# Kernel optimization log

Hardware: AMD Instinct MI355X
Metric: run time of the kernel (lower is better)

## Reference

```python
import jax, jax.numpy as jnp
import numpy as np

N_NODES = 50000


def _gcn_norm(edge_index):
    # symmetric GCN normalization 1/sqrt(deg_src*deg_dst), computed from edge list
    src, dst = edge_index[0], edge_index[1]
    ones = jnp.ones(src.shape[0], dtype=jnp.float32)
    deg = jax.ops.segment_sum(ones, dst, num_segments=N_NODES)
    deg = jnp.maximum(deg, 1.0)
    inv_sqrt = jax.lax.rsqrt(deg)
    return inv_sqrt[src] * inv_sqrt[dst]  # [E]


def _graph_conv(x, src, dst, norm, W, b):
    # gather messages from source nodes, normalize, scatter-add to destinations
    msgs = x[src] * norm[:, None]                       # [E, F]
    agg = jax.ops.segment_sum(msgs, dst, num_segments=N_NODES)  # [N, F]
    return agg @ W + b


def setup_inputs() -> dict:
    key = jax.random.key(0)
    ks = jax.random.split(key, 8)
    F, H, C, E = 128, 256, 40, 600000
    x = jax.random.normal(ks[0], (N_NODES, F), dtype=jnp.float32)
    edge_index = jax.random.randint(ks[1], (2, E), 0, N_NODES, dtype=jnp.int32)
    W1 = jax.random.normal(ks[2], (F, H), dtype=jnp.float32) * (1.0 / np.sqrt(F))
    b1 = jnp.zeros((H,), dtype=jnp.float32)
    W2 = jax.random.normal(ks[3], (H, H), dtype=jnp.float32) * (1.0 / np.sqrt(H))
    b2 = jnp.zeros((H,), dtype=jnp.float32)
    Wd = jax.random.normal(ks[4], (H, C), dtype=jnp.float32) * (1.0 / np.sqrt(H))
    bd = jnp.zeros((C,), dtype=jnp.float32)
    return {"x": x, "edge_index": edge_index, "W1": W1, "b1": b1,
            "W2": W2, "b2": b2, "Wd": Wd, "bd": bd}


def reference(x, edge_index, W1, b1, W2, b2, Wd, bd):
    src, dst = edge_index[0], edge_index[1]
    norm = _gcn_norm(edge_index)
    h = jax.nn.relu(_graph_conv(x, src, dst, norm, W1, b1))
    h = jax.nn.relu(_graph_conv(h, src, dst, norm, W2, b2))
    return jax.nn.softmax(h @ Wd + bd, axis=-1)
```

## Files before the change

### kernel.cpp

```cpp
#include <hip/hip_runtime.h>
#include <hip/hip_bf16.h>
#include <math.h>

#define N_NODES 50000

typedef short short8 __attribute__((ext_vector_type(8)));
typedef float f32x4 __attribute__((ext_vector_type(4)));

static __device__ __forceinline__ void split2(float x, unsigned short& hi, unsigned short& lo) {
    unsigned u = __builtin_bit_cast(unsigned, x);
    unsigned r = u + 0x7FFF + ((u >> 16) & 1);
    hi = (unsigned short)(r >> 16);
    float hf = __builtin_bit_cast(float, (unsigned)hi << 16);
    float res = x - hf;
    unsigned v = __builtin_bit_cast(unsigned, res);
    unsigned r2 = v + 0x7FFF + ((v >> 16) & 1);
    lo = (unsigned short)(r2 >> 16);
}


__global__ void deg_kernel(const int* __restrict__ dst, int* __restrict__ deg, int E) {
    int e = blockIdx.x * blockDim.x + threadIdx.x;
    if (e < E) atomicAdd(&deg[dst[e]], 1);
}


__global__ void scan_p1(const int* __restrict__ deg, int* __restrict__ bsum, int n) {
    int t = threadIdx.x;
    int base = blockIdx.x * 1024 + t * 4;
    int4 v = make_int4(0, 0, 0, 0);
    if (base + 3 < n) v = *(const int4*)(deg + base);
    else {
        if (base + 0 < n) v.x = deg[base + 0];
        if (base + 1 < n) v.y = deg[base + 1];
        if (base + 2 < n) v.z = deg[base + 2];
    }
    int s = v.x + v.y + v.z + v.w;
    #pragma unroll
    for (int off = 32; off > 0; off >>= 1) s += __shfl_xor(s, off);
    __shared__ int wpart[4];
    if ((t & 63) == 0) wpart[t >> 6] = s;
    __syncthreads();
    if (t == 0) bsum[blockIdx.x] = wpart[0] + wpart[1] + wpart[2] + wpart[3];
}

__global__ void scan_p2(int* __restrict__ bsum, int nb, int* __restrict__ rowptr, int n) {
    int t = threadIdx.x;
    int v = (t < nb) ? bsum[t] : 0;
    int sc = v;
    #pragma unroll
    for (int off = 1; off < 64; off <<= 1) {
        int u = __shfl_up(sc, off);
        if (t >= off) sc += u;
    }
    if (t < nb) bsum[t] = sc - v;
    if (t == 63) rowptr[n] = sc;
}

__global__ void scan_p3(const int* __restrict__ deg, const int* __restrict__ bsum,
                        int* __restrict__ rowptr, int* __restrict__ cursor,
                        float* __restrict__ inv, int n) {
    int t = threadIdx.x;
    int base = blockIdx.x * 1024 + t * 4;
    int4 v = make_int4(0, 0, 0, 0);
    if (base + 3 < n) v = *(const int4*)(deg + base);
    else {
        if (base + 0 < n) v.x = deg[base + 0];
        if (base + 1 < n) v.y = deg[base + 1];
        if (base + 2 < n) v.z = deg[base + 2];
    }
    int s = v.x + v.y + v.z + v.w;
    int lane = t & 63;
    int sc = s;
    #pragma unroll
    for (int off = 1; off < 64; off <<= 1) {
        int u = __shfl_up(sc, off);
        if (lane >= off) sc += u;
    }
    __shared__ int wpart[4], woff[4];
    if (lane == 63) wpart[t >> 6] = sc;
    __syncthreads();
    if (t == 0) { int a = 0; for (int i = 0; i < 4; ++i) { woff[i] = a; a += wpart[i]; } }
    __syncthreads();
    int run = bsum[blockIdx.x] + woff[t >> 6] + (sc - s);
    if (base + 0 < n) { rowptr[base + 0] = run; cursor[base + 0] = run; run += v.x; inv[base + 0] = rsqrtf(fmaxf((float)v.x, 1.0f)); }
    if (base + 1 < n) { rowptr[base + 1] = run; cursor[base + 1] = run; run += v.y; inv[base + 1] = rsqrtf(fmaxf((float)v.y, 1.0f)); }
    if (base + 2 < n) { rowptr[base + 2] = run; cursor[base + 2] = run; run += v.z; inv[base + 2] = rsqrtf(fmaxf((float)v.z, 1.0f)); }
    if (base + 3 < n) { rowptr[base + 3] = run; cursor[base + 3] = run; run += v.w; inv[base + 3] = rsqrtf(fmaxf((float)v.w, 1.0f)); }
}


__global__ void fill_kernel(const int* __restrict__ src, const int* __restrict__ dst,
                            const float* __restrict__ inv, int* __restrict__ cursor,
                            int* __restrict__ src_s, float* __restrict__ norm_s, int E) {
    int e = blockIdx.x * blockDim.x + threadIdx.x;
    if (e >= E) return;
    int s = src[e];
    int d = dst[e];
    int pos = atomicAdd(&cursor[d], 1);
    src_s[pos] = s;
    norm_s[pos] = inv[s] * inv[d];
}


__global__ void gather_agg_pass(const float* __restrict__ x, int coff, int ss,
                                const int* __restrict__ rowptr, const int* __restrict__ src_s,
                                const float* __restrict__ norm_s,
                                unsigned short* __restrict__ agg_hi,
                                unsigned short* __restrict__ agg_lo, int as) {
    int node = blockIdx.x * 4 + (threadIdx.x >> 6);
    if (node >= N_NODES) return;
    int lane = threadIdx.x & 63;
    int beg = rowptr[node];
    int end = rowptr[node + 1];
    const float* xb = x + coff + (size_t)lane * 2;

    float2 acc = {0.0f, 0.0f};
    int p = beg;
    for (; p + 4 <= end; p += 4) {
        int s0 = src_s[p], s1 = src_s[p + 1], s2 = src_s[p + 2], s3 = src_s[p + 3];
        float n0 = norm_s[p], n1 = norm_s[p + 1], n2 = norm_s[p + 2], n3 = norm_s[p + 3];
        float2 v0 = *(const float2*)(xb + (size_t)s0 * ss);
        float2 v1 = *(const float2*)(xb + (size_t)s1 * ss);
        float2 v2 = *(const float2*)(xb + (size_t)s2 * ss);
        float2 v3 = *(const float2*)(xb + (size_t)s3 * ss);
        acc.x = fmaf(v0.x, n0, acc.x); acc.y = fmaf(v0.y, n0, acc.y);
        acc.x = fmaf(v1.x, n1, acc.x); acc.y = fmaf(v1.y, n1, acc.y);
        acc.x = fmaf(v2.x, n2, acc.x); acc.y = fmaf(v2.y, n2, acc.y);
        acc.x = fmaf(v3.x, n3, acc.x); acc.y = fmaf(v3.y, n3, acc.y);
    }
    for (; p < end; ++p) {
        int s0 = src_s[p];
        float n0 = norm_s[p];
        float2 v0 = *(const float2*)(xb + (size_t)s0 * ss);
        acc.x = fmaf(v0.x, n0, acc.x);
        acc.y = fmaf(v0.y, n0, acc.y);
    }

    unsigned short h0, l0, h1, l1;
    split2(acc.x, h0, l0);
    split2(acc.y, h1, l1);
    unsigned hp = (unsigned)h0 | ((unsigned)h1 << 16);
    unsigned lp = (unsigned)l0 | ((unsigned)l1 << 16);
    size_t o = (size_t)node * as + coff + (size_t)lane * 2;
    *(unsigned*)(agg_hi + o) = hp;
    *(unsigned*)(agg_lo + o) = lp;
}


__global__ void split_w_all(const float* __restrict__ W1, const float* __restrict__ W2,
                            unsigned short* __restrict__ w1hi, unsigned short* __restrict__ w1lo,
                            unsigned short* __restrict__ w2hi, unsigned short* __restrict__ w2lo) {
    int i = blockIdx.x * 256 + threadIdx.x;
    if (i < 128 * 256) {
        int k = i >> 8;
        int n = i & 255;
        unsigned short h, l;
        split2(W1[i], h, l);
        w1hi[(size_t)n * 128 + k] = h;
        w1lo[(size_t)n * 128 + k] = l;
    } else {
        int j = i - 128 * 256;
        int k = j >> 8;
        int n = j & 255;
        unsigned short h, l;
        split2(W2[j], h, l);
        w2hi[(size_t)n * 256 + k] = h;
        w2lo[(size_t)n * 256 + k] = l;
    }
}


template<int K, bool RELU>
__global__ __launch_bounds__(256) void gemm_mfma_kernel(
    const unsigned short* __restrict__ Ahi, const unsigned short* __restrict__ Alo,
    const unsigned short* __restrict__ Bhi, const unsigned short* __restrict__ Blo,
    const float* __restrict__ bias, float* __restrict__ out, int M)
{
    constexpr int LDA = 40;
    __shared__ unsigned short AsH[2][64][LDA];
    __shared__ unsigned short AsL[2][64][LDA];

    int tid = threadIdx.x;
    int lane = tid & 63;
    int wave = tid >> 6;
    int row0 = blockIdx.x * 64;
    int col0 = wave * 64;
    int lr = lane & 15;
    int koff0 = (lane >> 4) * 8;

    int srow = tid >> 2;
    int skg = (tid & 3) << 3;

    f32x4 acc[4][4];
    #pragma unroll
    for (int i = 0; i < 4; ++i)
        #pragma unroll
        for (int j = 0; j < 4; ++j) acc[i][j] = (f32x4){0.f, 0.f, 0.f, 0.f};

    short8 rh, rl;
    rh = *(const short8*)(Ahi + (size_t)(row0 + srow) * K + skg);
    rl = *(const short8*)(Alo + (size_t)(row0 + srow) * K + skg);
    *(short8*)&AsH[0][srow][skg] = rh;
    *(short8*)&AsL[0][srow][skg] = rl;
    __syncthreads();

    constexpr int NT = K / 32;
    #pragma unroll 1
    for (int t = 0; t < NT; ++t) {
        int cur = t & 1;
        int ko = t * 32 + koff0;

        short8 bh[4], bl[4];
        #pragma unroll
        for (int q = 0; q < 4; ++q) {
            size_t boff = (size_t)(col0 + q * 16 + lr) * K + ko;
            bh[q] = *(const short8*)(Bhi + boff);
            bl[q] = *(const short8*)(Blo + boff);
        }

        if (t + 1 < NT) {
            int kk = (t + 1) * 32;
            rh = *(const short8*)(Ahi + (size_t)(row0 + srow) * K + kk + skg);
            rl = *(const short8*)(Alo + (size_t)(row0 + srow) * K + kk + skg);
        }

        short8 ah[4], al[4];
        #pragma unroll
        for (int q = 0; q < 4; ++q) {
            ah[q] = *(const short8*)&AsH[cur][q * 16 + lr][koff0];
            al[q] = *(const short8*)&AsL[cur][q * 16 + lr][koff0];
        }

        #pragma unroll
        for (int mt = 0; mt < 4; ++mt)
            #pragma unroll
            for (int nt = 0; nt < 4; ++nt) {
                acc[mt][nt] = __builtin_amdgcn_mfma_f32_16x16x32_bf16(ah[mt], bh[nt], acc[mt][nt], 0, 0, 0);
                acc[mt][nt] = __builtin_amdgcn_mfma_f32_16x16x32_bf16(ah[mt], bl[nt], acc[mt][nt], 0, 0, 0);
                acc[mt][nt] = __builtin_amdgcn_mfma_f32_16x16x32_bf16(al[mt], bh[nt], acc[mt][nt], 0, 0, 0);
            }

        if (t + 1 < NT) {
            *(short8*)&AsH[cur ^ 1][srow][skg] = rh;
            *(short8*)&AsL[cur ^ 1][srow][skg] = rl;
        }
        __syncthreads();
    }

    int rgrp = (lane >> 4) * 4;
    #pragma unroll
    for (int mt = 0; mt < 4; ++mt) {
        #pragma unroll
        for (int nt = 0; nt < 4; ++nt) {
            int c = col0 + nt * 16 + lr;
            float bv = bias[c];
            #pragma unroll
            for (int reg = 0; reg < 4; ++reg) {
                int r = row0 + mt * 16 + rgrp + reg;
                if (r < M) {
                    float v = acc[mt][nt][reg] + bv;
                    if (RELU) v = fmaxf(v, 0.0f);
                    out[(size_t)r * 256 + c] = v;
                }
            }
        }
    }
}


__global__ __launch_bounds__(256) void dense_softmax_kernel(const float* __restrict__ h,
                                                            const float* __restrict__ Wd,
                                                            const float* __restrict__ bd,
                                                            float* __restrict__ out, int M) {
    __shared__ float hs[32][260];
    __shared__ float wt[40][260];
    int tid = threadIdx.x;
    int row0 = blockIdx.x * 32;

    for (int i = tid; i < 40 * 256; i += 256) {
        int k = i / 40;
        int c = i - k * 40;
        wt[c][k] = Wd[i];
    }
    #pragma unroll
    for (int i = 0; i < 8; ++i) {
        int f = tid + i * 256;
        int r = f >> 6;
        int k4 = (f & 63) << 2;
        float4 v = make_float4(0.f, 0.f, 0.f, 0.f);
        if (row0 + r < M) v = *(const float4*)(h + (size_t)(row0 + r) * 256 + k4);
        *(float4*)&hs[r][k4] = v;
    }
    __syncthreads();

    int r  = tid >> 3;
    int cg = tid & 7;
    int c0 = cg * 5;

    float acc[5] = {0.f, 0.f, 0.f, 0.f, 0.f};
    #pragma unroll 4
    for (int k4 = 0; k4 < 64; ++k4) {
        float4 hv = *(float4*)&hs[r][k4 * 4];
        #pragma unroll
        for (int j = 0; j < 5; ++j) {
            float4 wv = *(float4*)&wt[c0 + j][k4 * 4];
            acc[j] = fmaf(hv.x, wv.x, acc[j]);
            acc[j] = fmaf(hv.y, wv.y, acc[j]);
            acc[j] = fmaf(hv.z, wv.z, acc[j]);
            acc[j] = fmaf(hv.w, wv.w, acc[j]);
        }
    }
    #pragma unroll
    for (int j = 0; j < 5; ++j) acc[j] += bd[c0 + j];

    float m = acc[0];
    #pragma unroll
    for (int j = 1; j < 5; ++j) m = fmaxf(m, acc[j]);
    #pragma unroll
    for (int off = 1; off < 8; off <<= 1) m = fmaxf(m, __shfl_xor(m, off));

    float e[5], s = 0.f;
    #pragma unroll
    for (int j = 0; j < 5; ++j) { e[j] = expf(acc[j] - m); s += e[j]; }
    #pragma unroll
    for (int off = 1; off < 8; off <<= 1) s += __shfl_xor(s, off);

    int row = row0 + r;
    if (row < M) {
        float inv_s = 1.0f / s;
        float* orow = out + (size_t)row * 40 + c0;
        #pragma unroll
        for (int j = 0; j < 5; ++j) orow[j] = e[j] * inv_s;
    }
}


extern "C" void kernel_launch(void* const* d_in, const int* in_sizes, int n_in,
                              void* d_out, int out_size, void* d_ws, size_t ws_size,
                              hipStream_t stream) {
    const float* x  = (const float*)d_in[0];
    const int*   ei = (const int*)d_in[1];
    const float* W1 = (const float*)d_in[2];
    const float* b1 = (const float*)d_in[3];
    const float* W2 = (const float*)d_in[4];
    const float* b2 = (const float*)d_in[5];
    const float* Wd = (const float*)d_in[6];
    const float* bd = (const float*)d_in[7];
    float* out = (float*)d_out;

    const int N = N_NODES;
    const int E = in_sizes[1] / 2;
    const int* src = ei;
    const int* dst = ei + E;

    const int MP = 50048;

    char* ws = (char*)d_ws;
    size_t off = 0;
    auto alloc = [&](size_t bytes) { char* p = ws + off; off += (bytes + 1023) & ~(size_t)1023; return p; };
    int*   deg    = (int*)alloc((size_t)N * 4);
    float* inv    = (float*)alloc((size_t)N * 4);
    int*   rowptr = (int*)alloc((size_t)(N + 1) * 4);
    int*   cursor = (int*)alloc((size_t)N * 4);
    int*   bsum   = (int*)alloc((size_t)64 * 4);
    int*   src_s  = (int*)alloc((size_t)E * 4);
    float* norm_s = (float*)alloc((size_t)E * 4);
    float* h1     = (float*)alloc((size_t)N * 256 * 4);
    unsigned short* aggU = (unsigned short*)alloc((size_t)MP * 256 * 2 * 2);
    unsigned short* w1hi = (unsigned short*)alloc((size_t)128 * 256 * 2);
    unsigned short* w1lo = (unsigned short*)alloc((size_t)128 * 256 * 2);
    unsigned short* w2hi = (unsigned short*)alloc((size_t)256 * 256 * 2);
    unsigned short* w2lo = (unsigned short*)alloc((size_t)256 * 256 * 2);

    unsigned short* agg1_hi = aggU;
    unsigned short* agg1_lo = aggU + (size_t)MP * 128;
    unsigned short* agg2_hi = aggU;
    unsigned short* agg2_lo = aggU + (size_t)MP * 256;
    float* h2 = h1;

    hipMemsetAsync(deg, 0, (size_t)N * 4, stream);

    const int nb = (N + 1023) / 1024;

    deg_kernel<<<(E + 255) / 256, 256, 0, stream>>>(dst, deg, E);
    scan_p1<<<nb, 256, 0, stream>>>(deg, bsum, N);
    scan_p2<<<1, 64, 0, stream>>>(bsum, nb, rowptr, N);
    scan_p3<<<nb, 256, 0, stream>>>(deg, bsum, rowptr, cursor, inv, N);
    fill_kernel<<<(E + 255) / 256, 256, 0, stream>>>(src, dst, inv, cursor, src_s, norm_s, E);

    split_w_all<<<(128 * 256 + 256 * 256) / 256, 256, 0, stream>>>(W1, W2, w1hi, w1lo, w2hi, w2lo);

    const int gblocks = (N + 3) / 4;

    gather_agg_pass<<<gblocks, 256, 0, stream>>>(x, 0, 128, rowptr, src_s, norm_s, agg1_hi, agg1_lo, 128);
    gemm_mfma_kernel<128, true><<<MP / 64, 256, 0, stream>>>(agg1_hi, agg1_lo, w1hi, w1lo, b1, h1, N);

    gather_agg_pass<<<gblocks, 256, 0, stream>>>(h1, 0,   256, rowptr, src_s, norm_s, agg2_hi, agg2_lo, 256);
    gather_agg_pass<<<gblocks, 256, 0, stream>>>(h1, 128, 256, rowptr, src_s, norm_s, agg2_hi, agg2_lo, 256);
    gemm_mfma_kernel<256, true><<<MP / 64, 256, 0, stream>>>(agg2_hi, agg2_lo, w2hi, w2lo, b2, h2, N);

    dense_softmax_kernel<<<(N + 31) / 32, 256, 0, stream>>>(h2, Wd, bd, out, N);
}
```

Before: 342.9 us.

## Halve GEMM row tile and swap MFMA operands for vectorized float4 stores

```diff
diff --git a/kernel.cpp b/kernel.cpp
--- a/kernel.cpp
+++ b/kernel.cpp
@@ -178,31 +178,33 @@
     const float* __restrict__ bias, float* __restrict__ out, int M)
 {
     constexpr int LDA = 40;
-    __shared__ unsigned short AsH[2][64][LDA];
-    __shared__ unsigned short AsL[2][64][LDA];
+    __shared__ unsigned short AsH[2][32][LDA];
+    __shared__ unsigned short AsL[2][32][LDA];
 
     int tid = threadIdx.x;
     int lane = tid & 63;
     int wave = tid >> 6;
-    int row0 = blockIdx.x * 64;
+    int row0 = blockIdx.x * 32;
     int col0 = wave * 64;
     int lr = lane & 15;
-    int koff0 = (lane >> 4) * 8;
-
-    int srow = tid >> 2;
-    int skg = (tid & 3) << 3;
-
-    f32x4 acc[4][4];
+    int lhi = lane >> 4;
+    int koff0 = lhi * 8;
+
+    int s = tid & 127;
+    int srow = s >> 2;
+    int skg = (s & 3) << 3;
+    const unsigned short* Astage = (tid < 128) ? Ahi : Alo;
+
+    f32x4 acc[4][2];
     #pragma unroll
     for (int i = 0; i < 4; ++i)
         #pragma unroll
-        for (int j = 0; j < 4; ++j) acc[i][j] = (f32x4){0.f, 0.f, 0.f, 0.f};
-
-    short8 rh, rl;
-    rh = *(const short8*)(Ahi + (size_t)(row0 + srow) * K + skg);
-    rl = *(const short8*)(Alo + (size_t)(row0 + srow) * K + skg);
-    *(short8*)&AsH[0][srow][skg] = rh;
-    *(short8*)&AsL[0][srow][skg] = rl;
+        for (int j = 0; j < 2; ++j) acc[i][j] = (f32x4){0.f, 0.f, 0.f, 0.f};
+
+    short8 rstage;
+    rstage = *(const short8*)(Astage + (size_t)(row0 + srow) * K + skg);
+    if (tid < 128) *(short8*)&AsH[0][srow][skg] = rstage;
+    else           *(short8*)&AsL[0][srow][skg] = rstage;
     __syncthreads();
 
     constexpr int NT = K / 32;
@@ -213,56 +215,57 @@
 
         short8 bh[4], bl[4];
         #pragma unroll
-        for (int q = 0; q < 4; ++q) {
-            size_t boff = (size_t)(col0 + q * 16 + lr) * K + ko;
-            bh[q] = *(const short8*)(Bhi + boff);
-            bl[q] = *(const short8*)(Blo + boff);
+        for (int cf = 0; cf < 4; ++cf) {
+            size_t boff = (size_t)(col0 + cf * 16 + lr) * K + ko;
+            bh[cf] = *(const short8*)(Bhi + boff);
+            bl[cf] = *(const short8*)(Blo + boff);
         }
 
         if (t + 1 < NT) {
-            int kk = (t + 1) * 32;
-            rh = *(const short8*)(Ahi + (size_t)(row0 + srow) * K + kk + skg);
-            rl = *(const short8*)(Alo + (size_t)(row0 + srow) * K + kk + skg);
-        }
-
-        short8 ah[4], al[4];
-        #pragma unroll
-        for (int q = 0; q < 4; ++q) {
-            ah[q] = *(const short8*)&AsH[cur][q * 16 + lr][koff0];
-            al[q] = *(const short8*)&AsL[cur][q * 16 + lr][koff0];
-        }
-
-        #pragma unroll
-        for (int mt = 0; mt < 4; ++mt)
+            rstage = *(const short8*)(Astage + (size_t)(row0 + srow) * K + (t + 1) * 32 + skg);
+        }
+
+        short8 ah[2], al[2];
+        #pragma unroll
+        for (int rf = 0; rf < 2; ++rf) {
+            ah[rf] = *(const short8*)&AsH[cur][rf * 16 + lr][koff0];
+            al[rf] = *(const short8*)&AsL[cur][rf * 16 + lr][koff0];
+        }
+
+        #pragma unroll
+        for (int cf = 0; cf < 4; ++cf)
             #pragma unroll
-            for (int nt = 0; nt < 4; ++nt) {
-                acc[mt][nt] = __builtin_amdgcn_mfma_f32_16x16x32_bf16(ah[mt], bh[nt], acc[mt][nt], 0, 0, 0);
-                acc[mt][nt] = __builtin_amdgcn_mfma_f32_16x16x32_bf16(ah[mt], bl[nt], acc[mt][nt], 0, 0, 0);
-                acc[mt][nt] = __builtin_amdgcn_mfma_f32_16x16x32_bf16(al[mt], bh[nt], acc[mt][nt], 0, 0, 0);
+            for (int rf = 0; rf < 2; ++rf) {
+                acc[cf][rf] = __builtin_amdgcn_mfma_f32_16x16x32_bf16(bh[cf], ah[rf], acc[cf][rf], 0, 0, 0);
+                acc[cf][rf] = __builtin_amdgcn_mfma_f32_16x16x32_bf16(bl[cf], ah[rf], acc[cf][rf], 0, 0, 0);
+                acc[cf][rf] = __builtin_amdgcn_mfma_f32_16x16x32_bf16(bh[cf], al[rf], acc[cf][rf], 0, 0, 0);
             }
 
         if (t + 1 < NT) {
-            *(short8*)&AsH[cur ^ 1][srow][skg] = rh;
-            *(short8*)&AsL[cur ^ 1][srow][skg] = rl;
+            if (tid < 128) *(short8*)&AsH[cur ^ 1][srow][skg] = rstage;
+            else           *(short8*)&AsL[cur ^ 1][srow][skg] = rstage;
         }
         __syncthreads();
     }
 
-    int rgrp = (lane >> 4) * 4;
-    #pragma unroll
-    for (int mt = 0; mt < 4; ++mt) {
-        #pragma unroll
-        for (int nt = 0; nt < 4; ++nt) {
-            int c = col0 + nt * 16 + lr;
-            float bv = bias[c];
-            #pragma unroll
-            for (int reg = 0; reg < 4; ++reg) {
-                int r = row0 + mt * 16 + rgrp + reg;
-                if (r < M) {
-                    float v = acc[mt][nt][reg] + bv;
-                    if (RELU) v = fmaxf(v, 0.0f);
-                    out[(size_t)r * 256 + c] = v;
+    #pragma unroll
+    for (int cf = 0; cf < 4; ++cf) {
+        int c = col0 + cf * 16 + lhi * 4;
+        float4 bv = *(const float4*)(bias + c);
+        #pragma unroll
+        for (int rf = 0; rf < 2; ++rf) {
+            int r = row0 + rf * 16 + lr;
+            if (r < M) {
+                float4 v;
+                v.x = acc[cf][rf][0] + bv.x;
+                v.y = acc[cf][rf][1] + bv.y;
+                v.z = acc[cf][rf][2] + bv.z;
+                v.w = acc[cf][rf][3] + bv.w;
+                if (RELU) {
+                    v.x = fmaxf(v.x, 0.f); v.y = fmaxf(v.y, 0.f);
+                    v.z = fmaxf(v.z, 0.f); v.w = fmaxf(v.w, 0.f);
                 }
+                *(float4*)(out + (size_t)r * 256 + c) = v;
             }
         }
     }
@@ -394,11 +397,11 @@
     const int gblocks = (N + 3) / 4;
 
     gather_agg_pass<<<gblocks, 256, 0, stream>>>(x, 0, 128, rowptr, src_s, norm_s, agg1_hi, agg1_lo, 128);
-    gemm_mfma_kernel<128, true><<<MP / 64, 256, 0, stream>>>(agg1_hi, agg1_lo, w1hi, w1lo, b1, h1, N);
+    gemm_mfma_kernel<128, true><<<MP / 32, 256, 0, stream>>>(agg1_hi, agg1_lo, w1hi, w1lo, b1, h1, N);
 
     gather_agg_pass<<<gblocks, 256, 0, stream>>>(h1, 0,   256, rowptr, src_s, norm_s, agg2_hi, agg2_lo, 256);
     gather_agg_pass<<<gblocks, 256, 0, stream>>>(h1, 128, 256, rowptr, src_s, norm_s, agg2_hi, agg2_lo, 256);
-    gemm_mfma_kernel<256, true><<<MP / 64, 256, 0, stream>>>(agg2_hi, agg2_lo, w2hi, w2lo, b2, h2, N);
+    gemm_mfma_kernel<256, true><<<MP / 32, 256, 0, stream>>>(agg2_hi, agg2_lo, w2hi, w2lo, b2, h2, N);
 
     dense_softmax_kernel<<<(N + 31) / 32, 256, 0, stream>>>(h2, Wd, bd, out, N);
 }
```

Result: slower. 357.4 us (+4.2%).
